# Optimization experiments

Measured on AMD Instinct MI355X. Metric: run time of the kernel, lower is better.

Reference implementation:

```python
import jax, jax.numpy as jnp
import numpy as np

D_MODEL = 2048
N_HEADS = 16
N_KV = 4
HEAD_DIM = 128
EPS = 1e-5


def _rmsnorm(x, w, eps=EPS):
    var = jnp.mean(x * x, axis=-1, keepdims=True)
    return x * jax.lax.rsqrt(var + eps) * w


def _rope_cos_sin(seq_len, head_dim, dtype):
    inv_freq = 1.0 / (10000.0 ** (jnp.arange(0, head_dim, 2, dtype=jnp.float32) / head_dim))
    t = jnp.arange(seq_len, dtype=jnp.float32)
    freqs = jnp.outer(t, inv_freq)  # [S, hd/2]
    return jnp.cos(freqs).astype(dtype), jnp.sin(freqs).astype(dtype)


def _apply_rope(x, cos, sin):
    # x: [B,H,S,hd]; cos/sin: [S,hd/2] broadcast as [1,1,S,hd/2]
    half = x.shape[-1] // 2
    x1, x2 = x[..., :half], x[..., half:]
    c = cos[None, None]
    s = sin[None, None]
    return jnp.concatenate([x1 * c - x2 * s, x1 * s + x2 * c], axis=-1)


def setup_inputs() -> dict:
    key = jax.random.key(0)
    ks = jax.random.split(key, 7)
    qkv_out = (N_HEADS + 2 * N_KV) * HEAD_DIM  # 3072
    d = D_MODEL
    inp = {
        "x": jax.random.normal(ks[0], (2, 2048, d), dtype=jnp.float32),
        "w_qkv": jax.random.normal(ks[1], (qkv_out, d), dtype=jnp.float32) * (1.0 / np.sqrt(d)),
        "q_norm_w": jnp.ones((HEAD_DIM,), dtype=jnp.float32),
        "k_norm_w": jnp.ones((HEAD_DIM,), dtype=jnp.float32),
        "w_gate": jax.random.normal(ks[2], (N_HEADS, d), dtype=jnp.float32) * 0.02,
        "b_gate": jnp.ones((N_HEADS,), dtype=jnp.float32),
        "w_o": jax.random.normal(ks[3], (d, N_HEADS * HEAD_DIM), dtype=jnp.float32) * (1.0 / np.sqrt(N_HEADS * HEAD_DIM)),
    }
    return inp


def reference(x, w_qkv, q_norm_w, k_norm_w, w_gate, b_gate, w_o):
    B, S, D = x.shape
    hd = HEAD_DIM
    scale = 1.0 / np.sqrt(hd)
    n_rep = N_HEADS // N_KV

    qkv = jnp.einsum("bsd,od->bso", x, w_qkv)  # [B,S,(H+2KV)*hd]
    q_size = N_HEADS * hd
    kv_size = N_KV * hd
    q = qkv[..., :q_size].reshape(B, S, N_HEADS, hd).transpose(0, 2, 1, 3)
    k = qkv[..., q_size:q_size + kv_size].reshape(B, S, N_KV, hd).transpose(0, 2, 1, 3)
    v = qkv[..., q_size + kv_size:].reshape(B, S, N_KV, hd).transpose(0, 2, 1, 3)

    q = _rmsnorm(q, q_norm_w)
    k = _rmsnorm(k, k_norm_w)

    cos, sin = _rope_cos_sin(S, hd, q.dtype)
    q = _apply_rope(q, cos, sin)
    k = _apply_rope(k, cos, sin)

    # GQA: repeat kv heads
    k = jnp.repeat(k, n_rep, axis=1)  # [B,H,S,hd]
    v = jnp.repeat(v, n_rep, axis=1)

    scores = jnp.einsum("bhqd,bhkd->bhqk", q, k) * scale
    causal = jnp.triu(jnp.ones((S, S), dtype=bool), k=1)
    neg = jnp.finfo(scores.dtype).min
    scores = jnp.where(causal[None, None], neg, scores)
    probs = jax.nn.softmax(scores, axis=-1)
    attn = jnp.einsum("bhqk,bhkd->bhqd", probs, v)  # [B,H,S,hd]

    # g1 gating on attention output per query head
    gate = jax.nn.sigmoid(jnp.einsum("bsd,hd->bsh", x, w_gate) + b_gate)  # [B,S,H]
    attn = attn * gate.transpose(0, 2, 1)[..., None]

    attn = attn.transpose(0, 2, 1, 3).reshape(B, S, N_HEADS * hd)
    out = jnp.einsum("bsf,df->bsd", attn, w_o)
    return out
```

## Files before the change

kernel.cpp:

```cpp
#include <hip/hip_runtime.h>

typedef __bf16 bf16x8 __attribute__((ext_vector_type(8)));
typedef float f32x4 __attribute__((ext_vector_type(4)));

typedef __attribute__((address_space(1))) void gvoid;
typedef __attribute__((address_space(3))) void lvoid;

__device__ __forceinline__ void gl_lds16(const void* g, void* l) {
    __builtin_amdgcn_global_load_lds((gvoid*)g, (lvoid*)l, 16, 0, 0);
}

__device__ __forceinline__ float fin(float v) {
    v = (v == v) ? v : 0.f;
    return fminf(fmaxf(v, -3.0e38f), 3.0e38f);
}

__device__ __forceinline__ bf16x8 cvt8(float4 a, float4 b) {
    bf16x8 r;
    r[0] = (__bf16)a.x; r[1] = (__bf16)a.y; r[2] = (__bf16)a.z; r[3] = (__bf16)a.w;
    r[4] = (__bf16)b.x; r[5] = (__bf16)b.y; r[6] = (__bf16)b.z; r[7] = (__bf16)b.w;
    return r;
}

__device__ __forceinline__ void cvt_range(const float* __restrict__ in,
                                          __bf16* __restrict__ out, int i) {
    const float4* p = (const float4*)in + (size_t)i * 2;
    ((bf16x8*)out)[i] = cvt8(p[0], p[1]);
}

__global__ __launch_bounds__(256) void prep_kernel(const float* __restrict__ x,
                                                   const float* __restrict__ wqkv,
                                                   __bf16* __restrict__ xb,
                                                   __bf16* __restrict__ wqb,
                                                   const float* __restrict__ wg,
                                                   const float* __restrict__ bg,
                                                   float* __restrict__ gate,
                                                   float2* __restrict__ ropet) {
    __shared__ float gp[4][16];
    int bid = blockIdx.x, tid = threadIdx.x;
    if (bid < 4096) {
        int lane = tid & 63, wave = tid >> 6;
        const float4* xr = (const float4*)(x + (size_t)bid * 2048);
        float4 p0 = xr[tid * 2], p1 = xr[tid * 2 + 1];
        ((bf16x8*)xb)[bid * 256 + tid] = cvt8(p0, p1);
#pragma unroll
        for (int h = 0; h < 16; ++h) {
            const float4* wr = (const float4*)(wg + (size_t)h * 2048);
            float4 w0 = wr[tid * 2], w1 = wr[tid * 2 + 1];
            float acc = p0.x * w0.x + p0.y * w0.y + p0.z * w0.z + p0.w * w0.w +
                        p1.x * w1.x + p1.y * w1.y + p1.z * w1.z + p1.w * w1.w;
#pragma unroll
            for (int m = 1; m < 64; m <<= 1) acc += __shfl_xor(acc, m);
            if (lane == 0) gp[wave][h] = acc;
        }
        __syncthreads();
        if (tid < 16) {
            int s = bid & 2047, b = bid >> 11;
            float z = gp[0][tid] + gp[1][tid] + gp[2][tid] + gp[3][tid] + bg[tid];
            gate[((size_t)b * 16 + tid) * 2048 + s] = 1.f / (1.f + __expf(-z));
        }
        return;
    }
    if (bid < 7168) {
        cvt_range(wqkv, wqb, (bid - 4096) * 256 + tid);
        return;
    }
    int idx = (bid - 7168) * 256 + tid;
    int s = idx >> 6, d0 = idx & 63;
    float freq = (float)s * __expf(-(float)d0 * (9.2103403719761836f / 64.0f));
    ropet[idx] = make_float2(cosf(freq), sinf(freq));
}

template <int WMT, int WNT, int EPI, typename TC>
__global__ __launch_bounds__(512) void gemm8p(const __bf16* __restrict__ A,
                                              const __bf16* __restrict__ B,
                                              TC* __restrict__ C,
                                              int M, int N, int K,
                                              const float* __restrict__ kw,
                                              const float2* __restrict__ ropet,
                                              __bf16* __restrict__ Kx) {
    constexpr int BM = WMT * 32;
    constexpr int BN = WNT * 64;
    constexpr int LA = BM / 128;
    constexpr int LB = BN / 128;
    constexpr int VMC = 2 * LA + LB;

    __shared__ __align__(16) __bf16 As[2][BM * 64];
    __shared__ __align__(16) __bf16 Bs[2][BN * 64];

    const int tid = threadIdx.x;
    const int lane = tid & 63, wave = tid >> 6;
    const int wm = wave >> 2, wn = wave & 3;
    const int quad = lane >> 4, mrow = lane & 15;

    const int nbx = gridDim.x;
    const int nwg = nbx * gridDim.y;
    const int orig = (int)blockIdx.y * nbx + (int)blockIdx.x;
    const int wg = (orig & 7) * (nwg >> 3) + (orig >> 3);
    const size_t row0 = (size_t)(wg / nbx) * BM;
    const size_t col0 = (size_t)(wg % nbx) * BN;

    size_t sA[LA], sB[LB];
    int dA[LA], dB[LB];
#pragma unroll
    for (int c = 0; c < LA; ++c) {
        int q = c * 512 + tid;
        int a = q * 16;
        int p = (a >> 4) & 63;
        int rowl = (a >> 11) * 16 + (p >> 2);
        int g = (p & 3) ^ ((p >> 3) & 3);
        int col = ((a >> 10) & 1) * 32 + g * 8;
        sA[c] = (size_t)rowl * K + col;
        dA[c] = q * 8;
    }
#pragma unroll
    for (int c = 0; c < LB; ++c) {
        int q = c * 512 + tid;
        int a = q * 16;
        int p = (a >> 4) & 63;
        int rowl = (a >> 11) * 16 + (p >> 2);
        int g = (p & 3) ^ ((p >> 3) & 3);
        int col = ((a >> 10) & 1) * 32 + g * 8;
        sB[c] = (size_t)rowl * K + col;
        dB[c] = q * 8;
    }

    const __bf16* Ag = A + row0 * K;
    const __bf16* Bg = B + col0 * K;

    f32x4 acc[WMT][WNT];
#pragma unroll
    for (int i = 0; i < WMT; ++i)
#pragma unroll
        for (int j = 0; j < WNT; ++j) acc[i][j] = (f32x4){0.f, 0.f, 0.f, 0.f};

    const int abase = mrow * 64 + ((quad ^ ((mrow >> 1) & 3)) * 16);

    bf16x8 af[WMT / 2][2], bf[WNT / 2][2];

#define STA8(buf, h, kt)                                                        \
    _Pragma("unroll") for (int c = 0; c < LA; ++c)                              \
        gl_lds16(Ag + (size_t)(h) * (BM / 2) * K + (size_t)(kt) * 64 + sA[c],   \
                 &As[buf][(h) * (BM / 2) * 64 + dA[c]])

#define STB8(buf, h, kt)                                                        \
    _Pragma("unroll") for (int c = 0; c < LB; ++c)                              \
        gl_lds16(Bg + (size_t)(h) * (BN / 2) * K + (size_t)(kt) * 64 + sB[c],   \
                 &Bs[buf][(h) * (BN / 2) * 64 + dB[c]])

#define LDA8(buf, mh)                                                           \
    _Pragma("unroll") for (int m2 = 0; m2 < WMT / 2; ++m2)                      \
    _Pragma("unroll") for (int s = 0; s < 2; ++s)                               \
        af[m2][s] = *(const bf16x8*)((const char*)&As[buf][0] +                 \
            ((((mh) * (WMT / 2) + m2) * 2 + wm) * 2 + s) * 1024 + abase)

#define LDB8(buf, nh)                                                           \
    _Pragma("unroll") for (int n2 = 0; n2 < WNT / 2; ++n2)                      \
    _Pragma("unroll") for (int s = 0; s < 2; ++s)                               \
        bf[n2][s] = *(const bf16x8*)((const char*)&Bs[buf][0] +                 \
            ((((nh) * (WNT / 2) + n2) * 4 + wn) * 2 + s) * 1024 + abase)

#define MMA8(mh, nh)                                                            \
    _Pragma("unroll") for (int m2 = 0; m2 < WMT / 2; ++m2)                      \
    _Pragma("unroll") for (int n2 = 0; n2 < WNT / 2; ++n2)                      \
    _Pragma("unroll") for (int s = 0; s < 2; ++s)                               \
        acc[(mh) * (WMT / 2) + m2][(nh) * (WNT / 2) + n2] =                     \
            __builtin_amdgcn_mfma_f32_16x16x32_bf16(                            \
                af[m2][s], bf[n2][s],                                           \
                acc[(mh) * (WMT / 2) + m2][(nh) * (WNT / 2) + n2], 0, 0, 0)

#define BAR8 __builtin_amdgcn_s_barrier()

#define WAITVM                                                                  \
    do {                                                                        \
        if constexpr (VMC == 6)                                                 \
            asm volatile("s_waitcnt vmcnt(6)" ::: "memory");                    \
        else                                                                    \
            asm volatile("s_waitcnt vmcnt(4)" ::: "memory");                    \
    } while (0)

#define PHASE_TAIL(mh, nh)                                                      \
    __builtin_amdgcn_s_barrier();                                               \
    asm volatile("s_waitcnt lgkmcnt(0)" ::: "memory");                          \
    __builtin_amdgcn_sched_barrier(0);                                          \
    __builtin_amdgcn_s_setprio(1);                                              \
    MMA8(mh, nh);                                                               \
    __builtin_amdgcn_s_setprio(0)

    const int NT = K / 64;

    STA8(0, 0, 0);
    STB8(0, 0, 0);
    STA8(0, 1, 0);
    STB8(0, 1, 0);
    STA8(1, 0, 1);
    STB8(1, 1, 1);
    STA8(1, 1, 1);
    WAITVM;
    BAR8;

    for (int i = 0; i < NT / 2; ++i) {
        const int u = 2 * i;
        const int k2 = (u + 2 < NT) ? u + 2 : NT - 1;
        const int k3 = (u + 3 < NT) ? u + 3 : NT - 1;
        LDA8(0, 0); LDB8(0, 0); STB8(1, 0, u + 1);
        PHASE_TAIL(0, 0); BAR8;
        LDB8(0, 1); STA8(0, 0, k2);
        PHASE_TAIL(0, 1); BAR8;
        LDA8(0, 1); STB8(0, 1, k2);
        PHASE_TAIL(1, 1); BAR8;
        LDB8(0, 0); STA8(0, 1, k2);
        PHASE_TAIL(1, 0); WAITVM; BAR8;
        LDA8(1, 0); LDB8(1, 0); STB8(0, 0, k2);
        PHASE_TAIL(0, 0); BAR8;
        LDB8(1, 1); STA8(1, 0, k3);
        PHASE_TAIL(0, 1); BAR8;
        LDA8(1, 1); STB8(1, 1, k3);
        PHASE_TAIL(1, 1); BAR8;
        LDB8(1, 0); STA8(1, 1, k3);
        PHASE_TAIL(1, 0); WAITVM; BAR8;
    }
    asm volatile("s_waitcnt vmcnt(0)" ::: "memory");

#undef STA8
#undef STB8
#undef LDA8
#undef LDB8
#undef MMA8
#undef BAR8
#undef WAITVM
#undef PHASE_TAIL

    if constexpr (EPI) {
        int xblk = (int)(col0 >> 8);
        if (xblk == 8 || xblk == 9) {
            __syncthreads();
            float* sums = (float*)&As[0][0];
            const int d0 = wn * 16 + mrow;
#pragma unroll
            for (int mt = 0; mt < WMT; ++mt)
#pragma unroll
                for (int t = 0; t < 2; ++t) {
                    f32x4 p;
#pragma unroll
                    for (int r = 0; r < 4; ++r)
                        p[r] = acc[mt][2 * t][r] * acc[mt][2 * t][r] +
                               acc[mt][2 * t + 1][r] * acc[mt][2 * t + 1][r];
#pragma unroll
                    for (int m = 1; m < 16; m <<= 1)
#pragma unroll
                        for (int r = 0; r < 4; ++r) p[r] += __shfl_xor(p[r], m);
                    if (mrow == 0) {
                        int idx = ((((wm * 8 + mt) * 4 + quad) * 2 + t) * 4 + wn) * 4;
#pragma unroll
                        for (int r = 0; r < 4; ++r) sums[idx + r] = p[r];
                    }
                }
            __syncthreads();
            float w1 = kw[d0], w2 = kw[d0 + 64];
#pragma unroll
            for (int mt = 0; mt < WMT; ++mt) {
                int rbase = (int)row0 + (mt * 2 + wm) * 16 + quad * 4;
#pragma unroll
                for (int t = 0; t < 2; ++t) {
                    int ib = (((wm * 8 + mt) * 4 + quad) * 2 + t) * 16;
                    f32x4 sv = *(const f32x4*)&sums[ib] + *(const f32x4*)&sums[ib + 4] +
                               *(const f32x4*)&sums[ib + 8] + *(const f32x4*)&sums[ib + 12];
                    int kvh = (xblk - 8) * 2 + t;
#pragma unroll
                    for (int r = 0; r < 4; ++r) {
                        int row = rbase + r;
                        int s_ = row & 2047, b_ = row >> 11;
                        float inv = rsqrtf(sv[r] * (1.0f / 128.0f) + 1e-5f);
                        float2 cs = ropet[s_ * 64 + d0];
                        float y1 = acc[mt][2 * t][r] * inv * w1;
                        float y2 = acc[mt][2 * t + 1][r] * inv * w2;
                        __bf16* dst = Kx + (((size_t)(b_ * 4 + kvh) * 2048 + s_) << 7);
                        dst[d0] = (__bf16)(y1 * cs.x - y2 * cs.y);
                        dst[d0 + 64] = (__bf16)(y1 * cs.y + y2 * cs.x);
                    }
                }
            }
            return;
        }
    }

#pragma unroll
    for (int mt = 0; mt < WMT; ++mt)
#pragma unroll
        for (int nt = 0; nt < WNT; ++nt)
#pragma unroll
            for (int r = 0; r < 4; ++r) {
                size_t row = row0 + (mt * 2 + wm) * 16 + quad * 4 + r;
                size_t col = col0 + (nt * 4 + wn) * 16 + mrow;
                C[row * N + col] = (TC)fin(acc[mt][nt][r]);
            }
}

#define SCALE_LOG2E 0.12751666797152713f

__global__ __launch_bounds__(256) void mid_kernel(const __bf16* __restrict__ qkv,
                                                  const float* __restrict__ qw,
                                                  const float2* __restrict__ ropet,
                                                  __bf16* __restrict__ Q,
                                                  __bf16* __restrict__ Vt) {
    __shared__ __align__(16) __bf16 tile[64][72];
    int bid = blockIdx.x, t = threadIdx.x;
    if (bid < 16384) {
        int wid = bid * 4 + (t >> 6);
        int lane = t & 63;
        int head = wid & 15;
        int bs = wid >> 4;
        int s = bs & 2047, b = bs >> 11;
        const __bf16* src = qkv + (size_t)bs * 3072 + head * 128;
        __bf16* dst = Q + ((size_t)(b * 16 + head) * 2048 + s) * 128;
        float x1 = (float)src[lane], x2 = (float)src[lane + 64];
        float ss = x1 * x1 + x2 * x2;
#pragma unroll
        for (int m = 1; m < 64; m <<= 1) ss += __shfl_xor(ss, m);
        float inv = rsqrtf(ss * (1.0f / 128.0f) + 1e-5f);
        float y1 = x1 * inv * qw[lane];
        float y2 = x2 * inv * qw[lane + 64];
        float2 cs = ropet[s * 64 + lane];
        dst[lane] = (__bf16)((y1 * cs.x - y2 * cs.y) * SCALE_LOG2E);
        dst[lane + 64] = (__bf16)((y1 * cs.y + y2 * cs.x) * SCALE_LOG2E);
        return;
    }
    int v = bid - 16384;
    int st0 = (v & 31) * 64;
    int dblk = (v >> 5) & 1;
    int bz = v >> 6;
    int b = bz >> 2, kv = bz & 3;
    const __bf16* src = qkv + (size_t)(b * 2048 + st0) * 3072 + 2560 + kv * 128 + dblk * 64;
#pragma unroll
    for (int it = 0; it < 2; ++it) {
        int row = it * 32 + (t >> 3);
        int ch = t & 7;
        *(bf16x8*)&tile[row][ch * 8] = *(const bf16x8*)(src + (size_t)row * 3072 + ch * 8);
    }
    __syncthreads();
    __bf16* dst = Vt + ((size_t)(b * 4 + kv) * 128 + dblk * 64) * 2048 + st0;
#pragma unroll
    for (int it = 0; it < 2; ++it) {
        int drow = it * 32 + (t >> 3);
        int sch = t & 7;
        bf16x8 vv;
#pragma unroll
        for (int j = 0; j < 8; ++j) vv[j] = tile[sch * 8 + j][drow];
        *(bf16x8*)(dst + (size_t)drow * 2048 + sch * 8) = vv;
    }
}

#define FIXED_M 20.0f

#define MFMA16(a, b, c) __builtin_amdgcn_mfma_f32_16x16x32_bf16(a, b, c, 0, 0, 0)

__device__ __forceinline__ int pswz(int e) { return e ^ (((e >> 7) & 1) << 4); }

template <int MODE>
__device__ __forceinline__ void attn_step(const __bf16* Kl, const __bf16* Vl,
                                          int ws, int quad, int mrow,
                                          const bf16x8* aq0, const bf16x8* aq1,
                                          f32x4* o0, f32x4* o1,
                                          f32x4& lf0, f32x4& lf1,
                                          __bf16* Pw) {
    bf16x8 ones;
#pragma unroll
    for (int i = 0; i < 8; ++i) ones[i] = (__bf16)1.0f;

    f32x4 sc0[4], sc1[4];
    __builtin_amdgcn_s_setprio(1);
#pragma unroll
    for (int jt = 0; jt < 4; ++jt) {
        f32x4 s0 = (f32x4){0.f, 0.f, 0.f, 0.f};
        f32x4 s1 = (f32x4){0.f, 0.f, 0.f, 0.f};
#pragma unroll
        for (int dt = 0; dt < 4; ++dt) {
            bf16x8 bk = *(const bf16x8*)&Kl[((dt * 4 + quad) * 64 + jt * 16 + mrow) * 8];
            if (MODE < 2) s0 = MFMA16(aq0[dt], bk, s0);
            s1 = MFMA16(aq1[dt], bk, s1);
        }
        sc0[jt] = s0;
        sc1[jt] = s1;
    }
    __builtin_amdgcn_s_setprio(0);

    if (MODE == 1) {
        int rloc = ws * 16 + quad * 4;
#pragma unroll
        for (int jt = 0; jt < 4; ++jt)
#pragma unroll
            for (int r = 0; r < 4; ++r)
                if (jt * 16 + mrow > rloc + r) sc0[jt][r] = -1e30f;
    }
    if (MODE == 2) {
        int rloc = ws * 16 + quad * 4;
#pragma unroll
        for (int jt = 0; jt < 4; ++jt)
#pragma unroll
            for (int r = 0; r < 4; ++r)
                if (jt * 16 + mrow > rloc + r) sc1[jt][r] = -1e30f;
    }

    const int rb0 = pswz(((0 * 4 + quad) * 16 + mrow) * 8);
    const int rb1 = pswz(((1 * 4 + quad) * 16 + mrow) * 8);
    bf16x8 ap0[2], ap1[2];
    if (MODE < 2) {
#pragma unroll
        for (int jt = 0; jt < 4; ++jt)
#pragma unroll
            for (int r = 0; r < 4; ++r) {
                float pv = exp2f(sc0[jt][r] - FIXED_M);
                int k = jt * 16 + mrow;
                Pw[pswz(((k >> 3) * 16 + quad * 4 + r) * 8 + (k & 7))] = (__bf16)pv;
            }
        ap0[0] = *(const bf16x8*)&Pw[rb0];
        ap0[1] = *(const bf16x8*)&Pw[rb1];
        lf0 = MFMA16(ap0[0], ones, lf0);
        lf0 = MFMA16(ap0[1], ones, lf0);
    }
#pragma unroll
    for (int jt = 0; jt < 4; ++jt)
#pragma unroll
        for (int r = 0; r < 4; ++r) {
            float pv = exp2f(sc1[jt][r] - FIXED_M);
            int k = jt * 16 + mrow;
            Pw[pswz(((k >> 3) * 16 + quad * 4 + r) * 8 + (k & 7))] = (__bf16)pv;
        }
    ap1[0] = *(const bf16x8*)&Pw[rb0];
    ap1[1] = *(const bf16x8*)&Pw[rb1];
    lf1 = MFMA16(ap1[0], ones, lf1);
    lf1 = MFMA16(ap1[1], ones, lf1);

    __builtin_amdgcn_s_setprio(1);
#pragma unroll
    for (int d2 = 0; d2 < 8; ++d2)
#pragma unroll
        for (int ks = 0; ks < 2; ++ks) {
            bf16x8 bv = *(const bf16x8*)&Vl[((ks * 4 + quad) * 128 + d2 * 16 + mrow) * 8];
            if (MODE < 2) o0[d2] = MFMA16(ap0[ks], bv, o0[d2]);
            o1[d2] = MFMA16(ap1[ks], bv, o1[d2]);
        }
    __builtin_amdgcn_s_setprio(0);
}

__global__ __launch_bounds__(512, 2) void attn_kernel(const __bf16* __restrict__ Q,
                                                      const __bf16* __restrict__ Kx,
                                                      const __bf16* __restrict__ Vt,
                                                      const float* __restrict__ gate,
                                                      __bf16* __restrict__ O,
                                                      const float* __restrict__ wo,
                                                      __bf16* __restrict__ wob) {
    __shared__ __align__(16) __bf16 Kl[2][2][64 * 128];
    __shared__ __align__(16) __bf16 Vl[2][2][128 * 64];
    __shared__ __align__(16) __bf16 Pl[8][1024];
    int tid = threadIdx.x, lane = tid & 63, wave = tid >> 6;

    if (blockIdx.x >= 512) {
        cvt_range(wo, wob, ((int)blockIdx.x - 512) * 512 + tid);
        return;
    }

    int ws = wave & 3, st = wave >> 2;
    int quad = lane >> 4, mrow = lane & 15;
    __bf16* Pw = &Pl[wave][0];

    int idx = blockIdx.x;
    int qb = 15 - (idx >> 5);
    int h = idx & 15, b = (idx >> 4) & 1;
    int kvh = h >> 2;

    int sst = tid >> 8, lt = tid & 255;
    const __bf16* kbase = Kx + (size_t)(b * 4 + kvh) * 2048 * 128 + (lt & 63) * 128 + (lt >> 6) * 8;
    const __bf16* vbase = Vt + (size_t)(b * 4 + kvh) * 128 * 2048 + (lt & 127) * 2048 + (lt >> 7) * 8;
    int ldst = lt * 8;

    auto STAGE = [&](int buf, int tile) {
        const __bf16* kp = kbase + (size_t)tile * 8192;
        const __bf16* vp = vbase + (size_t)tile * 64;
#pragma unroll
        for (int c = 0; c < 4; ++c) gl_lds16(kp + 32 * c, &Kl[sst][buf][ldst + 2048 * c]);
#pragma unroll
        for (int c = 0; c < 4; ++c) gl_lds16(vp + 16 * c, &Vl[sst][buf][ldst + 2048 * c]);
    };

    STAGE(0, sst);

    const __bf16* Qh = Q + ((size_t)(b * 16 + h) * 2048 + qb * 128 + ws * 16 + mrow) * 128;
    bf16x8 aq0[4], aq1[4];
#pragma unroll
    for (int dt = 0; dt < 4; ++dt) {
        aq0[dt] = *(const bf16x8*)(Qh + dt * 32 + quad * 8);
        aq1[dt] = *(const bf16x8*)(Qh + 8192 + dt * 32 + quad * 8);
    }

    f32x4 o0[8], o1[8];
#pragma unroll
    for (int d2 = 0; d2 < 8; ++d2) {
        o0[d2] = (f32x4){0.f, 0.f, 0.f, 0.f};
        o1[d2] = (f32x4){0.f, 0.f, 0.f, 0.f};
    }
    f32x4 lf0 = (f32x4){0.f, 0.f, 0.f, 0.f}, lf1 = (f32x4){0.f, 0.f, 0.f, 0.f};

    __syncthreads();

    int cur = 0;
    for (int kt = 0; kt < qb; ++kt) {
        STAGE(cur ^ 1, 2 * (kt + 1) + sst);
        attn_step<0>(Kl[st][cur], Vl[st][cur], ws, quad, mrow, aq0, aq1, o0, o1, lf0, lf1, Pw);
        __syncthreads();
        cur ^= 1;
    }
    if (st == 0)
        attn_step<1>(Kl[0][cur], Vl[0][cur], ws, quad, mrow, aq0, aq1, o0, o1, lf0, lf1, Pw);
    else
        attn_step<2>(Kl[1][cur], Vl[1][cur], ws, quad, mrow, aq0, aq1, o0, o1, lf0, lf1, Pw);

    __syncthreads();
    f32x4* mo = (f32x4*)&Kl[0][0][0];
    float* ml = (float*)&Pl[0][0];
    int mlane = ws * 64 + lane;
    if (st == 1) {
#pragma unroll
        for (int d2 = 0; d2 < 8; ++d2) {
            mo[d2 * 256 + mlane] = o0[d2];
            mo[(d2 + 8) * 256 + mlane] = o1[d2];
        }
#pragma unroll
        for (int r = 0; r < 4; ++r) {
            ml[r * 256 + mlane] = lf0[r];
            ml[(r + 4) * 256 + mlane] = lf1[r];
        }
    }
    __syncthreads();
    if (st == 0) {
#pragma unroll
        for (int d2 = 0; d2 < 8; ++d2) {
            o0[d2] += mo[d2 * 256 + mlane];
            o1[d2] += mo[(d2 + 8) * 256 + mlane];
        }
#pragma unroll
        for (int r = 0; r < 4; ++r) {
            lf0[r] += ml[r * 256 + mlane];
            lf1[r] += ml[(r + 4) * 256 + mlane];
        }
#pragma unroll
        for (int hf = 0; hf < 2; ++hf) {
            f32x4* oo = hf ? o1 : o0;
            f32x4 ll = hf ? lf1 : lf0;
            int srow0 = qb * 128 + hf * 64 + ws * 16 + quad * 4;
            float gv[4], il[4];
#pragma unroll
            for (int r = 0; r < 4; ++r) {
                gv[r] = gate[((size_t)b * 16 + h) * 2048 + srow0 + r];
                il[r] = 1.0f / fmaxf(ll[r], 1e-30f);
            }
#pragma unroll
            for (int d2 = 0; d2 < 8; ++d2)
#pragma unroll
                for (int r = 0; r < 4; ++r)
                    O[(size_t)(b * 2048 + srow0 + r) * 2048 + h * 128 + d2 * 16 + mrow] =
                        (__bf16)fin(oo[d2][r] * il[r] * gv[r]);
        }
    }
}

extern "C" void kernel_launch(void* const* d_in, const int* in_sizes, int n_in,
                              void* d_out, int out_size, void* d_ws, size_t ws_size,
                              hipStream_t stream) {
    const float* x = (const float*)d_in[0];
    const float* w_qkv = (const float*)d_in[1];
    const float* q_norm_w = (const float*)d_in[2];
    const float* k_norm_w = (const float*)d_in[3];
    const float* w_gate = (const float*)d_in[4];
    const float* b_gate = (const float*)d_in[5];
    const float* w_o = (const float*)d_in[6];
    float* out = (float*)d_out;

    char* ws = (char*)d_ws;
    char* od = (char*)d_out;
    __bf16* xb = (__bf16*)(od);
    __bf16* wqb = (__bf16*)(od + 16777216);
    float* gateb = (float*)(od + 29360128);
    float2* ropet = (float2*)(od + 29622272);
    __bf16* Qb = (__bf16*)(od);
    __bf16* qkv = (__bf16*)(ws);
    __bf16* attnb = (__bf16*)(ws);
    __bf16* wob = (__bf16*)(ws + 16777216);
    __bf16* Kb = (__bf16*)(ws + 25165824);
    __bf16* Vtb = (__bf16*)(ws + 29360128);

    prep_kernel<<<7680, 256, 0, stream>>>(x, w_qkv, xb, wqb, w_gate, b_gate, gateb, ropet);
    gemm8p<8, 4, 1, __bf16><<<dim3(3072 / 256, 4096 / 256), 512, 0, stream>>>(
        xb, wqb, qkv, 4096, 3072, 2048, k_norm_w, ropet, Kb);
    mid_kernel<<<16896, 256, 0, stream>>>(qkv, q_norm_w, ropet, Qb, Vtb);
    attn_kernel<<<1536, 512, 0, stream>>>(Qb, Kb, Vtb, gateb, attnb, w_o, wob);
    gemm8p<4, 4, 0, float><<<dim3(2048 / 256, 4096 / 128), 512, 0, stream>>>(
        attnb, wob, out, 4096, 2048, 2048, nullptr, nullptr, nullptr);
}
```

Before: 351.5 us.

## Fuse Q RMSNorm+RoPE into QKV GEMM epilogue and read Q in place

Moves the Q-head RMSNorm, RoPE and softmax scale into the QKV GEMM epilogue, which already handled K. This removes the separate Q pass in mid_kernel and the extra Q buffer round trip. Attention now reads Q directly from the strided qkv buffer and writes its output back into that buffer. The output GEMM consumes it with a new leading-dimension parameter. The w_o conversion moves out of the attention grid into its own kernel, which adds a launch but avoids idle extra blocks in attention.

```diff
diff --git a/kernel.cpp b/kernel.cpp
--- a/kernel.cpp
+++ b/kernel.cpp
@@ -27,6 +27,8 @@
     const float4* p = (const float4*)in + (size_t)i * 2;
     ((bf16x8*)out)[i] = cvt8(p[0], p[1]);
 }
+
+#define SCALE_LOG2E 0.12751666797152713f
 
 __global__ __launch_bounds__(256) void prep_kernel(const float* __restrict__ x,
                                                    const float* __restrict__ wqkv,
@@ -71,11 +73,17 @@
     ropet[idx] = make_float2(cosf(freq), sinf(freq));
 }
 
+__global__ __launch_bounds__(256) void wo_cvt_kernel(const float* __restrict__ wo,
+                                                     __bf16* __restrict__ wob) {
+    cvt_range(wo, wob, blockIdx.x * 256 + threadIdx.x);
+}
+
 template <int WMT, int WNT, int EPI, typename TC>
 __global__ __launch_bounds__(512) void gemm8p(const __bf16* __restrict__ A,
                                               const __bf16* __restrict__ B,
                                               TC* __restrict__ C,
-                                              int M, int N, int K,
+                                              int M, int N, int K, int ldA,
+                                              const float* __restrict__ qw,
                                               const float* __restrict__ kw,
                                               const float2* __restrict__ ropet,
                                               __bf16* __restrict__ Kx) {
@@ -110,7 +118,7 @@
         int rowl = (a >> 11) * 16 + (p >> 2);
         int g = (p & 3) ^ ((p >> 3) & 3);
         int col = ((a >> 10) & 1) * 32 + g * 8;
-        sA[c] = (size_t)rowl * K + col;
+        sA[c] = (size_t)rowl * ldA + col;
         dA[c] = q * 8;
     }
 #pragma unroll
@@ -125,7 +133,7 @@
         dB[c] = q * 8;
     }
 
-    const __bf16* Ag = A + row0 * K;
+    const __bf16* Ag = A + row0 * ldA;
     const __bf16* Bg = B + col0 * K;
 
     f32x4 acc[WMT][WNT];
@@ -140,7 +148,7 @@
 
 #define STA8(buf, h, kt)                                                        \
     _Pragma("unroll") for (int c = 0; c < LA; ++c)                              \
-        gl_lds16(Ag + (size_t)(h) * (BM / 2) * K + (size_t)(kt) * 64 + sA[c],   \
+        gl_lds16(Ag + (size_t)(h) * (BM / 2) * ldA + (size_t)(kt) * 64 + sA[c], \
                  &As[buf][(h) * (BM / 2) * 64 + dA[c]])
 
 #define STB8(buf, h, kt)                                                        \
@@ -233,7 +241,7 @@
 
     if constexpr (EPI) {
         int xblk = (int)(col0 >> 8);
-        if (xblk == 8 || xblk == 9) {
+        if (xblk < 10) {
             __syncthreads();
             float* sums = (float*)&As[0][0];
             const int d0 = wn * 16 + mrow;
@@ -257,7 +265,10 @@
                     }
                 }
             __syncthreads();
-            float w1 = kw[d0], w2 = kw[d0 + 64];
+            const bool isQ = (xblk < 8);
+            const float* w = isQ ? qw : kw;
+            float w1 = w[d0], w2 = w[d0 + 64];
+            float osc = isQ ? SCALE_LOG2E : 1.0f;
 #pragma unroll
             for (int mt = 0; mt < WMT; ++mt) {
                 int rbase = (int)row0 + (mt * 2 + wm) * 16 + quad * 4;
@@ -266,7 +277,6 @@
                     int ib = (((wm * 8 + mt) * 4 + quad) * 2 + t) * 16;
                     f32x4 sv = *(const f32x4*)&sums[ib] + *(const f32x4*)&sums[ib + 4] +
                                *(const f32x4*)&sums[ib + 8] + *(const f32x4*)&sums[ib + 12];
-                    int kvh = (xblk - 8) * 2 + t;
 #pragma unroll
                     for (int r = 0; r < 4; ++r) {
                         int row = rbase + r;
@@ -275,9 +285,18 @@
                         float2 cs = ropet[s_ * 64 + d0];
                         float y1 = acc[mt][2 * t][r] * inv * w1;
                         float y2 = acc[mt][2 * t + 1][r] * inv * w2;
-                        __bf16* dst = Kx + (((size_t)(b_ * 4 + kvh) * 2048 + s_) << 7);
-                        dst[d0] = (__bf16)(y1 * cs.x - y2 * cs.y);
-                        dst[d0 + 64] = (__bf16)(y1 * cs.y + y2 * cs.x);
+                        float v1 = (y1 * cs.x - y2 * cs.y) * osc;
+                        float v2 = (y1 * cs.y + y2 * cs.x) * osc;
+                        if (isQ) {
+                            size_t base = (size_t)row * N + col0 + (2 * t) * 64 + d0;
+                            C[base] = (TC)v1;
+                            C[base + 64] = (TC)v2;
+                        } else {
+                            int kvh = (xblk - 8) * 2 + t;
+                            __bf16* dst = Kx + (((size_t)(b_ * 4 + kvh) * 2048 + s_) << 7);
+                            dst[d0] = (__bf16)v1;
+                            dst[d0 + 64] = (__bf16)v2;
+                        }
                     }
                 }
             }
@@ -297,36 +316,10 @@
             }
 }
 
-#define SCALE_LOG2E 0.12751666797152713f
-
 __global__ __launch_bounds__(256) void mid_kernel(const __bf16* __restrict__ qkv,
-                                                  const float* __restrict__ qw,
-                                                  const float2* __restrict__ ropet,
-                                                  __bf16* __restrict__ Q,
                                                   __bf16* __restrict__ Vt) {
     __shared__ __align__(16) __bf16 tile[64][72];
-    int bid = blockIdx.x, t = threadIdx.x;
-    if (bid < 16384) {
-        int wid = bid * 4 + (t >> 6);
-        int lane = t & 63;
-        int head = wid & 15;
-        int bs = wid >> 4;
-        int s = bs & 2047, b = bs >> 11;
-        const __bf16* src = qkv + (size_t)bs * 3072 + head * 128;
-        __bf16* dst = Q + ((size_t)(b * 16 + head) * 2048 + s) * 128;
-        float x1 = (float)src[lane], x2 = (float)src[lane + 64];
-        float ss = x1 * x1 + x2 * x2;
-#pragma unroll
-        for (int m = 1; m < 64; m <<= 1) ss += __shfl_xor(ss, m);
-        float inv = rsqrtf(ss * (1.0f / 128.0f) + 1e-5f);
-        float y1 = x1 * inv * qw[lane];
-        float y2 = x2 * inv * qw[lane + 64];
-        float2 cs = ropet[s * 64 + lane];
-        dst[lane] = (__bf16)((y1 * cs.x - y2 * cs.y) * SCALE_LOG2E);
-        dst[lane + 64] = (__bf16)((y1 * cs.y + y2 * cs.x) * SCALE_LOG2E);
-        return;
-    }
-    int v = bid - 16384;
+    int v = blockIdx.x, t = threadIdx.x;
     int st0 = (v & 31) * 64;
     int dblk = (v >> 5) & 1;
     int bz = v >> 6;
@@ -444,23 +437,15 @@
     __builtin_amdgcn_s_setprio(0);
 }
 
-__global__ __launch_bounds__(512, 2) void attn_kernel(const __bf16* __restrict__ Q,
+__global__ __launch_bounds__(512, 2) void attn_kernel(__bf16* __restrict__ qkvO,
                                                       const __bf16* __restrict__ Kx,
                                                       const __bf16* __restrict__ Vt,
-                                                      const float* __restrict__ gate,
-                                                      __bf16* __restrict__ O,
-                                                      const float* __restrict__ wo,
-                                                      __bf16* __restrict__ wob) {
+                                                      const float* __restrict__ gate) {
     __shared__ __align__(16) __bf16 Kl[2][2][64 * 128];
     __shared__ __align__(16) __bf16 Vl[2][2][128 * 64];
     __shared__ __align__(16) __bf16 Pl[8][1024];
     int tid = threadIdx.x, lane = tid & 63, wave = tid >> 6;
 
-    if (blockIdx.x >= 512) {
-        cvt_range(wo, wob, ((int)blockIdx.x - 512) * 512 + tid);
-        return;
-    }
-
     int ws = wave & 3, st = wave >> 2;
     int quad = lane >> 4, mrow = lane & 15;
     __bf16* Pw = &Pl[wave][0];
@@ -486,12 +471,12 @@
 
     STAGE(0, sst);
 
-    const __bf16* Qh = Q + ((size_t)(b * 16 + h) * 2048 + qb * 128 + ws * 16 + mrow) * 128;
+    const __bf16* Qh = qkvO + (size_t)(b * 2048 + qb * 128 + ws * 16 + mrow) * 3072 + h * 128;
     bf16x8 aq0[4], aq1[4];
 #pragma unroll
     for (int dt = 0; dt < 4; ++dt) {
         aq0[dt] = *(const bf16x8*)(Qh + dt * 32 + quad * 8);
-        aq1[dt] = *(const bf16x8*)(Qh + 8192 + dt * 32 + quad * 8);
+        aq1[dt] = *(const bf16x8*)(Qh + (size_t)64 * 3072 + dt * 32 + quad * 8);
     }
 
     f32x4 o0[8], o1[8];
@@ -559,7 +544,7 @@
             for (int d2 = 0; d2 < 8; ++d2)
 #pragma unroll
                 for (int r = 0; r < 4; ++r)
-                    O[(size_t)(b * 2048 + srow0 + r) * 2048 + h * 128 + d2 * 16 + mrow] =
+                    qkvO[(size_t)(b * 2048 + srow0 + r) * 3072 + h * 128 + d2 * 16 + mrow] =
                         (__bf16)fin(oo[d2][r] * il[r] * gv[r]);
         }
     }
@@ -583,18 +568,17 @@
     __bf16* wqb = (__bf16*)(od + 16777216);
     float* gateb = (float*)(od + 29360128);
     float2* ropet = (float2*)(od + 29622272);
-    __bf16* Qb = (__bf16*)(od);
     __bf16* qkv = (__bf16*)(ws);
-    __bf16* attnb = (__bf16*)(ws);
-    __bf16* wob = (__bf16*)(ws + 16777216);
     __bf16* Kb = (__bf16*)(ws + 25165824);
     __bf16* Vtb = (__bf16*)(ws + 29360128);
+    __bf16* wob = (__bf16*)(ws + 25165824);
 
     prep_kernel<<<7680, 256, 0, stream>>>(x, w_qkv, xb, wqb, w_gate, b_gate, gateb, ropet);
     gemm8p<8, 4, 1, __bf16><<<dim3(3072 / 256, 4096 / 256), 512, 0, stream>>>(
-        xb, wqb, qkv, 4096, 3072, 2048, k_norm_w, ropet, Kb);
-    mid_kernel<<<16896, 256, 0, stream>>>(qkv, q_norm_w, ropet, Qb, Vtb);
-    attn_kernel<<<1536, 512, 0, stream>>>(Qb, Kb, Vtb, gateb, attnb, w_o, wob);
+        xb, wqb, qkv, 4096, 3072, 2048, 2048, q_norm_w, k_norm_w, ropet, Kb);
+    mid_kernel<<<512, 256, 0, stream>>>(qkv, Vtb);
+    attn_kernel<<<512, 512, 0, stream>>>(qkv, Kb, Vtb, gateb);
+    wo_cvt_kernel<<<2048, 256, 0, stream>>>(w_o, wob);
     gemm8p<4, 4, 0, float><<<dim3(2048 / 256, 4096 / 128), 512, 0, stream>>>(
-        attnb, wob, out, 4096, 2048, 2048, nullptr, nullptr, nullptr);
-}
+        qkv, wob, out, 4096, 2048, 2048, 3072, nullptr, nullptr, nullptr, nullptr);
+}
```

Result: no change. 355.5 us (+1.1%).
